# Optimization experiments

Hardware: AMD Instinct MI355X
Metric: run time of the kernel (lower is better)

The kernel has to match this reference:

```python
import jax, jax.numpy as jnp
import numpy as np

H, DK, DV = 16, 64, 64
PHASE_MAX = 5
TEMP = 5.0
GAMMA = 0.9
BASE = 10000.0

def _rotate_half(x):
    d = x.shape[-1] // 2
    return jnp.concatenate((-x[..., d:], x[..., :d]), axis=-1)

def _inv_freq(dtype):
    return (1.0 / BASE ** (jnp.arange(0, DK, 2, dtype=jnp.float32) / DK)).astype(dtype)

def setup_inputs() -> dict:
    key = jax.random.key(0)
    ks = jax.random.split(key, 6)
    B, T, D = 4, 4096, 2048
    return {
        'hidden_states': jax.random.normal(ks[0], (B, T, D), jnp.float32),
        'W_turn': jax.random.normal(ks[1], (B, H, DV, DK), jnp.float32) * 0.1,
        'q_w': jax.random.normal(ks[2], (H * DK, D), jnp.float32) * 0.02,
        'o_w': jax.random.normal(ks[3], (D, H * DV), jnp.float32) * 0.02,
        'k_w': jax.random.normal(ks[4], (H * DK, D), jnp.float32) * 0.02,
        'v_w': jax.random.normal(ks[5], (H * DV, D), jnp.float32) * 0.02,
        'read_scale': jnp.asarray(-3.0, jnp.float32),
    }

def reference(hidden_states, W_turn, q_w, o_w, k_w, v_w, read_scale):
    B, T, D = hidden_states.shape
    dtype = hidden_states.dtype
    inv_freq = _inv_freq(dtype)

    # ---- read (layer 0) ----
    q = (hidden_states @ q_w.T).reshape(B, T, H, DK).transpose(0, 2, 1, 3)  # (B,H,T,dk)
    qn = jnp.linalg.norm(q, axis=-1, keepdims=True)
    q = q / jnp.maximum(qn, 1e-12)
    P = PHASE_MAX + 1
    phase = jnp.arange(P, dtype=dtype)
    angles = phase[:, None] * inv_freq                      # (P, dk/2)
    cos = jnp.concatenate([jnp.cos(angles)] * 2, axis=-1)   # (P, dk)
    sin = jnp.concatenate([jnp.sin(angles)] * 2, axis=-1)
    cos_b = cos.reshape(P, 1, 1, 1, DK)
    sin_b = sin.reshape(P, 1, 1, 1, DK)
    q_un = q[None]                                          # (P,B,H,T,dk)
    q_all = q_un * cos_b + _rotate_half(q_un) * sin_b
    reads = jnp.einsum('pbhtd,bhvd->pbhtv', q_all, W_turn)  # (P,B,H,T,dv)
    scores = jnp.linalg.norm(reads, axis=-1) / jnp.sqrt(jnp.asarray(DV, dtype))
    alpha = jax.nn.softmax(scores * TEMP, axis=0)           # (P,B,H,T)
    read = jnp.sum(alpha[..., None] * reads, axis=0)        # (B,H,T,dv)
    merged = read.transpose(0, 2, 1, 3).reshape(B, T, H * DV)
    out = hidden_states + jax.nn.sigmoid(read_scale).astype(dtype) * (merged @ o_w.T)

    # ---- write from content (content = hidden_states) ----
    k = (hidden_states @ k_w.T).reshape(B, T, H, DK).transpose(0, 2, 1, 3)
    v = (hidden_states @ v_w.T).reshape(B, T, H, DV).transpose(0, 2, 1, 3)
    kn = jnp.linalg.norm(k, axis=-1, keepdims=True)
    k = k / jnp.maximum(kn, 1e-12)
    residual = jnp.einsum('bhtv,bhtd->bhvd', v, k) / max(T, 1)
    cos1 = jnp.concatenate([jnp.cos(inv_freq)] * 2, axis=-1)  # 1-step aging
    sin1 = jnp.concatenate([jnp.sin(inv_freq)] * 2, axis=-1)
    W_aged = W_turn * cos1 + _rotate_half(W_turn) * sin1
    W_new = GAMMA * W_aged + residual
    return out, W_new
```

## Files before the change

### kernel.cpp

```cpp
#include <hip/hip_runtime.h>
#include <math.h>

typedef unsigned short u16;
typedef __bf16 bf16x8 __attribute__((ext_vector_type(8)));
typedef float f32x4 __attribute__((ext_vector_type(4)));

typedef __attribute__((address_space(1))) const void gas_t;
typedef __attribute__((address_space(3))) void las_t;

__device__ __forceinline__ void async16(const void* g, void* l) {
    __builtin_amdgcn_global_load_lds((gas_t*)g, (las_t*)l, 16, 0, 0);
}

__device__ __forceinline__ float b2f(u16 u) {
    union { unsigned u; float f; } c; c.u = ((unsigned)u) << 16; return c.f;
}
__device__ __forceinline__ u16 f2b(float f) {
    union { float f; unsigned u; } c; c.f = f;
    unsigned x = c.u + 0x7FFFu + ((c.u >> 16) & 1u);
    return (u16)(x >> 16);
}

__global__ __launch_bounds__(256)
void cvt_kernel(const float* __restrict__ in, u16* __restrict__ out, int n4) {
    int i = blockIdx.x * 256 + threadIdx.x;
    int stride = gridDim.x * 256;
    for (; i < n4; i += stride) {
        float4 f = ((const float4*)in)[i];
        ushort4 u;
        u.x = f2b(f.x); u.y = f2b(f.y); u.z = f2b(f.z); u.w = f2b(f.w);
        ((ushort4*)out)[i] = u;
    }
}

__global__ __launch_bounds__(256)
void cvt3_kernel(const float* __restrict__ a, const float* __restrict__ b,
                 const float* __restrict__ c, u16* __restrict__ out) {
    int i = blockIdx.x * 256 + threadIdx.x;
    int seg = i / 524288, off = i - seg * 524288;
    const float* src = (seg == 0) ? a : (seg == 1) ? b : c;
    float4 f = ((const float4*)src)[off];
    ushort4 u;
    u.x = f2b(f.x); u.y = f2b(f.y); u.z = f2b(f.z); u.w = f2b(f.w);
    ((ushort4*)out)[i] = u;
}

__global__ __launch_bounds__(256)
void wprep_kernel(const float* __restrict__ W, u16* __restrict__ wp) {
    int idx = blockIdx.x * 256 + threadIdx.x;
    int d = idx & 63;
    int v = (idx >> 6) & 63;
    int p = (idx >> 12) % 6;
    int bh = idx / 24576;
    const float* Wb = W + (((size_t)bh * 64 + v) << 6);
    float invf = expf(-(float)(d & 31) * (9.210340371976184f / 32.f));
    float ang = (float)p * invf;
    float c = cosf(ang), s = sinf(ang);
    float rot = (d < 32) ? Wb[d + 32] : -Wb[d - 32];
    wp[idx] = f2b(c * Wb[d] + s * rot);
}

template<int MODE>
__global__ __launch_bounds__(512, 2)
void gemm_bt128(const u16* __restrict__ A, const u16* __restrict__ Bw,
                int M, int N, int K,
                u16* __restrict__ obf, const float* __restrict__ resid,
                float* __restrict__ of32, const float* __restrict__ scale_ptr) {
    __shared__ __align__(16) u16 ls[3][24576];
    const int tid = threadIdx.x;
    const int lane = tid & 63;
    const int wm = (tid >> 6) >> 2;
    const int wn = (tid >> 6) & 3;
    const int nbx = N >> 8;

    int bid = blockIdx.x;
    const int cpx = gridDim.x >> 3;
    bid = (bid & 7) * cpx + (bid >> 3);
    const int m0 = (bid / nbx) << 7;
    const int n0 = (bid % nbx) << 8;

    f32x4 acc[4][4];
#pragma unroll
    for (int i = 0; i < 4; ++i)
#pragma unroll
        for (int j = 0; j < 4; ++j) acc[i][j] = (f32x4){0.f, 0.f, 0.f, 0.f};

    const int srow = tid >> 3;
    const int sslot = (tid & 7) ^ (srow & 7);
    const char* Ab = (const char*)A;
    const char* Bb = (const char*)Bw;
    const int nkt = K >> 6;

    auto stage = [&](int slot, int kt) {
        const int k0 = kt << 6;
        char* base = (char*)&ls[slot][0];
#pragma unroll
        for (int i = 0; i < 2; ++i) {
            int rowA = m0 + i * 64 + srow;
            async16(Ab + ((size_t)rowA * K + k0) * 2 + (sslot << 4),
                    base + i * 8192 + tid * 16);
        }
#pragma unroll
        for (int i = 0; i < 4; ++i) {
            int rowB = n0 + i * 64 + srow;
            async16(Bb + ((size_t)rowB * K + k0) * 2 + (sslot << 4),
                    base + 16384 + i * 8192 + tid * 16);
        }
    };

    stage(0, 0);
    stage(1, 1);
    for (int kt = 0; kt < nkt; ++kt) {
        if (kt < nkt - 1) asm volatile("s_waitcnt vmcnt(6)" ::: "memory");
        else              asm volatile("s_waitcnt vmcnt(0)" ::: "memory");
        __builtin_amdgcn_s_barrier();
        if (kt + 2 < nkt) stage((kt + 2) % 3, kt + 2);

        const char* Al = (const char*)&ls[kt % 3][0];
        const char* Bl = Al + 16384;
#pragma unroll
        for (int kk = 0; kk < 2; ++kk) {
            const int kb = kk * 64 + ((lane >> 4) << 4);
            bf16x8 af[4], bf[4];
#pragma unroll
            for (int m = 0; m < 4; ++m) {
                int row = wm * 64 + m * 16 + (lane & 15);
                af[m] = *(const bf16x8*)(Al + row * 128 + (kb ^ ((row & 7) << 4)));
            }
#pragma unroll
            for (int n = 0; n < 4; ++n) {
                int row = wn * 64 + n * 16 + (lane & 15);
                bf[n] = *(const bf16x8*)(Bl + row * 128 + (kb ^ ((row & 7) << 4)));
            }
            __builtin_amdgcn_s_setprio(1);
#pragma unroll
            for (int m = 0; m < 4; ++m)
#pragma unroll
                for (int n = 0; n < 4; ++n)
                    acc[m][n] = __builtin_amdgcn_mfma_f32_16x16x32_bf16(bf[n], af[m], acc[m][n], 0, 0, 0);
            __builtin_amdgcn_s_setprio(0);
        }
    }

    float sig = 0.f;
    if (MODE == 1) sig = 1.f / (1.f + expf(-scale_ptr[0]));

    const int crow = wm * 64 + (lane & 15);
    const int ccol0 = wn * 64 + ((lane >> 4) << 2);
#pragma unroll
    for (int m = 0; m < 4; ++m) {
#pragma unroll
        for (int n = 0; n < 4; ++n) {
            size_t gi = (size_t)(m0 + crow + m * 16) * N + (n0 + ccol0 + n * 16);
            if (MODE == 0) {
                ushort4 u;
                u.x = f2b(acc[m][n][0]); u.y = f2b(acc[m][n][1]);
                u.z = f2b(acc[m][n][2]); u.w = f2b(acc[m][n][3]);
                *(ushort4*)&obf[gi] = u;
            } else {
                float4 rv = *(const float4*)&resid[gi];
                float4 o;
                o.x = rv.x + sig * acc[m][n][0];
                o.y = rv.y + sig * acc[m][n][1];
                o.z = rv.z + sig * acc[m][n][2];
                o.w = rv.w + sig * acc[m][n][3];
                *(float4*)&of32[gi] = o;
            }
        }
    }
}

__global__ __launch_bounds__(256)
void reads_kernel(const u16* __restrict__ qkv, const u16* __restrict__ wp,
                  u16* __restrict__ merged) {
    __shared__ __align__(16) u16 lsW[384 * 64];
    const int tid = threadIdx.x, lane = tid & 63, w = tid >> 6;
    const int bh = blockIdx.x, tc = blockIdx.y;
    const int b = bh >> 4, h = bh & 15;

    const char* src = (const char*)(wp + (size_t)bh * 24576);
#pragma unroll
    for (int it = 0; it < 12; ++it) {
        int x = (it * 256 + tid) << 4;
        int row = x >> 7;
        int wb = x & 127;
        *(uint4*)((char*)lsW + x) = *(const uint4*)(src + row * 128 + (wb ^ ((row & 7) << 4)));
    }
    __syncthreads();

    for (int tt = 0; tt < 4; ++tt) {
        const int t0 = tc * 256 + tt * 64 + w * 16;
        const size_t qoff = ((size_t)b * 4096 + t0 + (lane & 15)) * 3072 + h * 64 + ((lane >> 4) << 3);
        uint4 a0u = *(const uint4*)&qkv[qoff];
        uint4 a1u = *(const uint4*)&qkv[qoff + 32];

        float ss = 0.f;
        {
            unsigned a[8] = {a0u.x, a0u.y, a0u.z, a0u.w, a1u.x, a1u.y, a1u.z, a1u.w};
#pragma unroll
            for (int i = 0; i < 8; ++i) {
                union { unsigned u; float f; } lo, hi;
                lo.u = a[i] << 16; hi.u = a[i] & 0xFFFF0000u;
                ss += lo.f * lo.f + hi.f * hi.f;
            }
        }
        ss += __shfl_xor(ss, 16);
        ss += __shfl_xor(ss, 32);
        float sc = 1.0f / fmaxf(sqrtf(ss), 1e-12f);

        bf16x8 a0 = __builtin_bit_cast(bf16x8, a0u);
        bf16x8 a1 = __builtin_bit_cast(bf16x8, a1u);

        f32x4 acc[24];
#pragma unroll
        for (int i = 0; i < 24; ++i) acc[i] = (f32x4){0.f, 0.f, 0.f, 0.f};
#pragma unroll
        for (int kk = 0; kk < 2; ++kk) {
            bf16x8 a = kk ? a1 : a0;
            const int kb = kk * 64 + ((lane >> 4) << 4);
#pragma unroll
            for (int nf = 0; nf < 24; ++nf) {
                int row = nf * 16 + (lane & 15);
                bf16x8 bb = *(const bf16x8*)((const char*)lsW + row * 128 + (kb ^ ((row & 7) << 4)));
                acc[nf] = __builtin_amdgcn_mfma_f32_16x16x32_bf16(bb, a, acc[nf], 0, 0, 0);
            }
        }

        float alpha[6];
#pragma unroll
        for (int p = 0; p < 6; ++p) {
            float x = 0.f;
#pragma unroll
            for (int fv = 0; fv < 4; ++fv) {
                f32x4 v = acc[p * 4 + fv];
#pragma unroll
                for (int r = 0; r < 4; ++r) x += v[r] * v[r];
            }
            x += __shfl_xor(x, 16);
            x += __shfl_xor(x, 32);
            alpha[p] = sqrtf(x) * sc * (5.0f / 8.0f);
        }
        {
            float m = alpha[0];
#pragma unroll
            for (int p = 1; p < 6; ++p) m = fmaxf(m, alpha[p]);
            float s = 0.f;
#pragma unroll
            for (int p = 0; p < 6; ++p) { float e = expf(alpha[p] - m); s += e; alpha[p] = e; }
            float inv = 1.f / s;
#pragma unroll
            for (int p = 0; p < 6; ++p) alpha[p] *= inv;
        }
#pragma unroll
        for (int fv = 0; fv < 4; ++fv) {
            float o[4];
#pragma unroll
            for (int r = 0; r < 4; ++r) {
                float acc_o = 0.f;
#pragma unroll
                for (int p = 0; p < 6; ++p) acc_o += alpha[p] * acc[p * 4 + fv][r];
                o[r] = acc_o * sc;
            }
            size_t gi = ((size_t)b * 4096 + t0 + (lane & 15)) * 1024
                        + h * 64 + fv * 16 + ((lane >> 4) << 2);
            ushort4 u;
            u.x = f2b(o[0]); u.y = f2b(o[1]); u.z = f2b(o[2]); u.w = f2b(o[3]);
            *(ushort4*)&merged[gi] = u;
        }
    }
}

__global__ __launch_bounds__(256)
void resid_mfma(const u16* __restrict__ qkv, float* __restrict__ part) {
    __shared__ __align__(16) u16 kT[64 * 32];
    __shared__ __align__(16) u16 vT[64 * 32];
    const int bh = blockIdx.x, sp = blockIdx.y;
    const int b = bh >> 4, h = bh & 15;
    const int tid = threadIdx.x, lane = tid & 63, wv = tid >> 6;
    const int tl = tid >> 3;
    const int c8 = tid & 7;

    f32x4 acc[4];
#pragma unroll
    for (int dt = 0; dt < 4; ++dt) acc[dt] = (f32x4){0.f, 0.f, 0.f, 0.f};

    const int r15 = lane & 15, g = lane >> 4;
    const int vrow = wv * 16 + r15;
    const int vaddr = vrow * 64 + ((g ^ ((vrow >> 3) & 3)) << 4);
    int kaddr[4];
#pragma unroll
    for (int dt = 0; dt < 4; ++dt) {
        int kr = dt * 16 + r15;
        kaddr[dt] = kr * 64 + ((g ^ ((kr >> 3) & 3)) << 4);
    }

    for (int c = 0; c < 8; ++c) {
        size_t row = ((size_t)b * 4096 + sp * 256 + c * 32 + tl) * 3072 + h * 64 + c8 * 8;
        uint4 kq = *(const uint4*)&qkv[row + 1024];
        uint4 vq = *(const uint4*)&qkv[row + 2048];

        unsigned kw[4] = {kq.x, kq.y, kq.z, kq.w};
        unsigned vw[4] = {vq.x, vq.y, vq.z, vq.w};
        float kf[8];
        float ss = 0.f;
#pragma unroll
        for (int i = 0; i < 4; ++i) {
            union { unsigned u; float f; } lo, hi;
            lo.u = kw[i] << 16; hi.u = kw[i] & 0xFFFF0000u;
            kf[2 * i] = lo.f; kf[2 * i + 1] = hi.f;
            ss += lo.f * lo.f + hi.f * hi.f;
        }
        ss += __shfl_xor(ss, 1);
        ss += __shfl_xor(ss, 2);
        ss += __shfl_xor(ss, 4);
        float sc = 1.0f / fmaxf(sqrtf(ss), 1e-12f);

        const int gt = (tl >> 3), o = (tl & 7);
#pragma unroll
        for (int j = 0; j < 8; ++j) {
            int r = 8 * c8 + j;
            int a = r * 32 + ((gt ^ ((r >> 3) & 3)) * 8 + o);
            kT[a] = f2b(kf[j] * sc);
            vT[a] = (u16)((vw[j >> 1] >> ((j & 1) * 16)) & 0xFFFFu);
        }
        __syncthreads();

        bf16x8 vf = *(const bf16x8*)((const char*)vT + vaddr);
#pragma unroll
        for (int dt = 0; dt < 4; ++dt) {
            bf16x8 knf = *(const bf16x8*)((const char*)kT + kaddr[dt]);
            acc[dt] = __builtin_amdgcn_mfma_f32_16x16x32_bf16(knf, vf, acc[dt], 0, 0, 0);
        }
        __syncthreads();
    }

    float* dst = part + ((size_t)sp * 64 + bh) * 4096 + (size_t)vrow * 64;
#pragma unroll
    for (int dt = 0; dt < 4; ++dt) {
        float4 f4;
        f4.x = acc[dt][0]; f4.y = acc[dt][1]; f4.z = acc[dt][2]; f4.w = acc[dt][3];
        *(float4*)(dst + dt * 16 + g * 4) = f4;
    }
}

__global__ __launch_bounds__(256)
void wnew_kernel(const float* __restrict__ W, const float* __restrict__ part,
                 float* __restrict__ outW) {
    int idx = blockIdx.x * 256 + threadIdx.x;
    int d = idx & 63;
    float w = W[idx];
    float rot = (d < 32) ? -W[idx + 32] : W[idx - 32];
    float invf = expf(-(float)(d & 31) * (9.210340371976184f / 32.f));
    float aged = w * cosf(invf) + rot * sinf(invf);
    float r = 0.f;
#pragma unroll
    for (int s = 0; s < 16; ++s) r += part[(size_t)s * 262144 + idx];
    outW[idx] = 0.9f * aged + r * (1.0f / 4096.0f);
}

extern "C" void kernel_launch(void* const* d_in, const int* in_sizes, int n_in,
                              void* d_out, int out_size, void* d_ws, size_t ws_size,
                              hipStream_t stream) {
    const float* hidden = (const float*)d_in[0];
    const float* Wturn  = (const float*)d_in[1];
    const float* qw     = (const float*)d_in[2];
    const float* ow     = (const float*)d_in[3];
    const float* kw     = (const float*)d_in[4];
    const float* vw     = (const float*)d_in[5];
    const float* rs     = (const float*)d_in[6];
    float* out  = (float*)d_out;
    float* outW = out + 33554432;

    char* ws = (char*)d_ws;
    u16* hid_bf = (u16*)(ws + 0);
    u16* qkv    = (u16*)(ws + 67108864);
    u16* mrg    = (u16*)(ws + 167772160);
    u16* wcat   = (u16*)(ws + 201326592);
    u16* ow_bf  = (u16*)(ws + 213909504);
    u16* wp     = (u16*)(ws + 218103808);
    float* part = (float*)(ws + 222298112);

    cvt_kernel<<<4096, 256, 0, stream>>>(hidden, hid_bf, 33554432 / 4);
    cvt3_kernel<<<6144, 256, 0, stream>>>(qw, kw, vw, wcat);
    cvt_kernel<<<2048, 256, 0, stream>>>(ow, ow_bf, 2097152 / 4);
    wprep_kernel<<<6144, 256, 0, stream>>>(Wturn, wp);

    gemm_bt128<0><<<1536, 512, 0, stream>>>(hid_bf, wcat, 16384, 3072, 2048, qkv, nullptr, nullptr, nullptr);

    reads_kernel<<<dim3(64, 16), 256, 0, stream>>>(qkv, wp, mrg);
    gemm_bt128<1><<<1024, 512, 0, stream>>>(mrg, ow_bf, 16384, 2048, 1024, nullptr, hidden, out, rs);
    resid_mfma<<<dim3(64, 16), 256, 0, stream>>>(qkv, part);
    wnew_kernel<<<1024, 256, 0, stream>>>(Wturn, part, outW);
}
```

Before: 457.4 us.

## Enlarge GEMM tile to 256x256 with half-K double-buffered phased staging

Replaces the 128x256 GEMM with a 256x256 block tile, so each wave accumulates 8x4 MFMA fragments. K tiles are staged in 32-wide halves into a double-buffered 128KB LDS area, with the next tile's loads interleaved between the two MFMA phases. The goal is more data reuse per LDS byte and better overlap of global loads with compute. In exchange, register pressure doubles, LDS use is much larger (one block per CU may fit despite the launch bound of 2), and the grid halves, which may hurt occupancy and tail balance.

```diff
diff --git a/kernel.cpp b/kernel.cpp
--- a/kernel.cpp
+++ b/kernel.cpp
@@ -62,82 +62,98 @@
 
 template<int MODE>
 __global__ __launch_bounds__(512, 2)
-void gemm_bt128(const u16* __restrict__ A, const u16* __restrict__ Bw,
-                int M, int N, int K,
-                u16* __restrict__ obf, const float* __restrict__ resid,
-                float* __restrict__ of32, const float* __restrict__ scale_ptr) {
-    __shared__ __align__(16) u16 ls[3][24576];
+void gemm_8ph(const u16* __restrict__ A, const u16* __restrict__ Bw,
+              int M, int N, int K,
+              u16* __restrict__ obf, const float* __restrict__ resid,
+              float* __restrict__ of32, const float* __restrict__ scale_ptr) {
+    __shared__ __align__(16) char lsb[2][65536];
     const int tid = threadIdx.x;
     const int lane = tid & 63;
     const int wm = (tid >> 6) >> 2;
     const int wn = (tid >> 6) & 3;
+    const int r15 = lane & 15;
     const int nbx = N >> 8;
 
     int bid = blockIdx.x;
     const int cpx = gridDim.x >> 3;
     bid = (bid & 7) * cpx + (bid >> 3);
-    const int m0 = (bid / nbx) << 7;
+    const int m0 = (bid / nbx) << 8;
     const int n0 = (bid % nbx) << 8;
 
-    f32x4 acc[4][4];
-#pragma unroll
-    for (int i = 0; i < 4; ++i)
+    f32x4 acc[8][4];
+#pragma unroll
+    for (int i = 0; i < 8; ++i)
 #pragma unroll
         for (int j = 0; j < 4; ++j) acc[i][j] = (f32x4){0.f, 0.f, 0.f, 0.f};
 
-    const int srow = tid >> 3;
-    const int sslot = (tid & 7) ^ (srow & 7);
     const char* Ab = (const char*)A;
     const char* Bb = (const char*)Bw;
+    const int ssl = (((tid & 3) ^ ((tid >> 3) & 3)) << 4);
+    const int slotRd = ((((lane >> 4) ^ ((r15 >> 1) & 3))) << 4);
     const int nkt = K >> 6;
 
-    auto stage = [&](int slot, int kt) {
-        const int k0 = kt << 6;
-        char* base = (char*)&ls[slot][0];
+    auto stage_half = [&](int buf, int mat, int kh, int kt) {
+        const char* src = mat ? Bb : Ab;
+        const int b0 = mat ? n0 : m0;
+        char* dst = &lsb[buf][0] + mat * 32768 + kh * 16384;
+        const int k0 = kt * 64 + kh * 32;
 #pragma unroll
         for (int i = 0; i < 2; ++i) {
-            int rowA = m0 + i * 64 + srow;
-            async16(Ab + ((size_t)rowA * K + k0) * 2 + (sslot << 4),
-                    base + i * 8192 + tid * 16);
-        }
-#pragma unroll
-        for (int i = 0; i < 4; ++i) {
-            int rowB = n0 + i * 64 + srow;
-            async16(Bb + ((size_t)rowB * K + k0) * 2 + (sslot << 4),
-                    base + 16384 + i * 8192 + tid * 16);
+            int row = i * 128 + (tid >> 2);
+            async16(src + ((size_t)(b0 + row) * K + k0) * 2 + ssl,
+                    dst + i * 8192 + tid * 16);
         }
     };
 
-    stage(0, 0);
-    stage(1, 1);
+    stage_half(0, 0, 0, 0);
+    stage_half(0, 1, 0, 0);
+    stage_half(0, 0, 1, 0);
+    stage_half(0, 1, 1, 0);
+
     for (int kt = 0; kt < nkt; ++kt) {
-        if (kt < nkt - 1) asm volatile("s_waitcnt vmcnt(6)" ::: "memory");
-        else              asm volatile("s_waitcnt vmcnt(0)" ::: "memory");
-        __builtin_amdgcn_s_barrier();
-        if (kt + 2 < nkt) stage((kt + 2) % 3, kt + 2);
-
-        const char* Al = (const char*)&ls[kt % 3][0];
-        const char* Bl = Al + 16384;
-#pragma unroll
-        for (int kk = 0; kk < 2; ++kk) {
-            const int kb = kk * 64 + ((lane >> 4) << 4);
-            bf16x8 af[4], bf[4];
+        const int cur = kt & 1;
+        const char* base = &lsb[cur][0];
+#pragma unroll
+        for (int kh = 0; kh < 2; ++kh) {
+            if (kt < nkt - 1) asm volatile("s_waitcnt vmcnt(4)" ::: "memory");
+            else if (kh == 0) asm volatile("s_waitcnt vmcnt(0)" ::: "memory");
+            __builtin_amdgcn_s_barrier();
+            if (kt + 1 < nkt) stage_half(cur ^ 1, 0, kh, kt + 1);
+
+            const char* Ak = base + kh * 16384;
+            const char* Bk = base + 32768 + kh * 16384;
+            bf16x8 bf[4], afl[4];
+#pragma unroll
+            for (int n = 0; n < 4; ++n) {
+                int row = wn * 64 + n * 16 + r15;
+                bf[n] = *(const bf16x8*)(Bk + row * 64 + slotRd);
+            }
 #pragma unroll
             for (int m = 0; m < 4; ++m) {
-                int row = wm * 64 + m * 16 + (lane & 15);
-                af[m] = *(const bf16x8*)(Al + row * 128 + (kb ^ ((row & 7) << 4)));
-            }
-#pragma unroll
-            for (int n = 0; n < 4; ++n) {
-                int row = wn * 64 + n * 16 + (lane & 15);
-                bf[n] = *(const bf16x8*)(Bl + row * 128 + (kb ^ ((row & 7) << 4)));
+                int row = wm * 128 + m * 16 + r15;
+                afl[m] = *(const bf16x8*)(Ak + row * 64 + slotRd);
             }
             __builtin_amdgcn_s_setprio(1);
 #pragma unroll
             for (int m = 0; m < 4; ++m)
 #pragma unroll
                 for (int n = 0; n < 4; ++n)
-                    acc[m][n] = __builtin_amdgcn_mfma_f32_16x16x32_bf16(bf[n], af[m], acc[m][n], 0, 0, 0);
+                    acc[m][n] = __builtin_amdgcn_mfma_f32_16x16x32_bf16(bf[n], afl[m], acc[m][n], 0, 0, 0);
+            __builtin_amdgcn_s_setprio(0);
+
+            if (kt + 1 < nkt) stage_half(cur ^ 1, 1, kh, kt + 1);
+            bf16x8 afh[4];
+#pragma unroll
+            for (int m = 0; m < 4; ++m) {
+                int row = wm * 128 + 64 + m * 16 + r15;
+                afh[m] = *(const bf16x8*)(Ak + row * 64 + slotRd);
+            }
+            __builtin_amdgcn_s_setprio(1);
+#pragma unroll
+            for (int m = 0; m < 4; ++m)
+#pragma unroll
+                for (int n = 0; n < 4; ++n)
+                    acc[4 + m][n] = __builtin_amdgcn_mfma_f32_16x16x32_bf16(bf[n], afh[m], acc[4 + m][n], 0, 0, 0);
             __builtin_amdgcn_s_setprio(0);
         }
     }
@@ -145,10 +161,10 @@
     float sig = 0.f;
     if (MODE == 1) sig = 1.f / (1.f + expf(-scale_ptr[0]));
 
-    const int crow = wm * 64 + (lane & 15);
+    const int crow = wm * 128 + r15;
     const int ccol0 = wn * 64 + ((lane >> 4) << 2);
 #pragma unroll
-    for (int m = 0; m < 4; ++m) {
+    for (int m = 0; m < 8; ++m) {
 #pragma unroll
         for (int n = 0; n < 4; ++n) {
             size_t gi = (size_t)(m0 + crow + m * 16) * N + (n0 + ccol0 + n * 16);
@@ -385,10 +401,10 @@
     cvt_kernel<<<2048, 256, 0, stream>>>(ow, ow_bf, 2097152 / 4);
     wprep_kernel<<<6144, 256, 0, stream>>>(Wturn, wp);
 
-    gemm_bt128<0><<<1536, 512, 0, stream>>>(hid_bf, wcat, 16384, 3072, 2048, qkv, nullptr, nullptr, nullptr);
+    gemm_8ph<0><<<768, 512, 0, stream>>>(hid_bf, wcat, 16384, 3072, 2048, qkv, nullptr, nullptr, nullptr);
 
     reads_kernel<<<dim3(64, 16), 256, 0, stream>>>(qkv, wp, mrg);
-    gemm_bt128<1><<<1024, 512, 0, stream>>>(mrg, ow_bf, 16384, 2048, 1024, nullptr, hidden, out, rs);
+    gemm_8ph<1><<<512, 512, 0, stream>>>(mrg, ow_bf, 16384, 2048, 1024, nullptr, hidden, out, rs);
     resid_mfma<<<dim3(64, 16), 256, 0, stream>>>(qkv, part);
     wnew_kernel<<<1024, 256, 0, stream>>>(Wturn, part, outW);
 }
```

Result: faster. 430.6 us (-5.9%).
